# Kernel optimization log

Measured on AMD Instinct MI355X. Metric: run time of the kernel, lower is better.

## Reference

```python
import jax, jax.numpy as jnp
import numpy as np

H = 12
DH = 64
R = 8
LN_EPS = 1e-12


def setup_inputs() -> dict:
    key = jax.random.key(0)
    ks = jax.random.split(key, 6)
    B, T, D = 32, 512, 768
    s = 0.02  # realistic init scale so softmax/LN stay well-conditioned
    return {
        "hidden_states": jax.random.normal(ks[0], (B, T, D), jnp.float32),
        "Wq": jax.random.normal(ks[1], (D, D), jnp.float32) * s,
        "bq": jnp.zeros((D,), jnp.float32),
        "Wk": jax.random.normal(ks[2], (D, D), jnp.float32) * s,
        "bk": jnp.zeros((D,), jnp.float32),
        "Wv": jax.random.normal(ks[3], (D, D), jnp.float32) * s,
        "bv": jnp.zeros((D,), jnp.float32),
        "Wo": jax.random.normal(ks[4], (D, D), jnp.float32) * s,
        "bo": jnp.zeros((D,), jnp.float32),
        "ln_g": jnp.ones((D,), jnp.float32),
        "ln_b": jnp.zeros((D,), jnp.float32),
    }


def _bipartite_indices(metric, r):
    # metric: (B, T, dh); cosine-sim bipartite matching between even (a) and odd (b) tokens
    m = metric / (jnp.linalg.norm(metric, axis=-1, keepdims=True) + 1e-6)
    a, b = m[:, ::2], m[:, 1::2]
    scores = jnp.einsum('bad,bcd->bac', a, b)  # (B, Ta, Tb)
    node_max = scores.max(axis=-1)
    node_idx = scores.argmax(axis=-1)
    node_max = node_max.at[:, 0].set(-jnp.inf)  # protect CLS (a[0])
    r = min(r, a.shape[1] - 1)
    sorted_idx = jnp.argsort(-node_max, axis=-1)  # descending
    src_idx = sorted_idx[:, :r]
    unm_idx = sorted_idx[:, r:]
    dst_idx = jnp.take_along_axis(node_idx, src_idx, axis=-1)
    return src_idx, unm_idx, dst_idx


def _merge(x, src_idx, unm_idx, dst_idx):
    # x: (B, T, C) -> (B, T - r, C); scatter-mean matched even tokens into odd tokens
    src, dst = x[:, ::2], x[:, 1::2]
    matched = jnp.take_along_axis(src, src_idx[:, :, None], axis=1)  # (B, r, C)

    def scat(d, di, mm):
        sums = jnp.zeros_like(d).at[di].add(mm)
        cnt = jnp.zeros((d.shape[0],), d.dtype).at[di].add(jnp.ones(di.shape, d.dtype))
        # torch scatter_reduce 'mean' with include_self=True: (self + sum) / (1 + count)
        return (d + sums) / (1.0 + cnt[:, None])

    dst = jax.vmap(scat)(dst, dst_idx, matched)
    unm = jnp.take_along_axis(src, unm_idx[:, :, None], axis=1)
    return jnp.concatenate([unm, dst], axis=1)


def reference(hidden_states, Wq, bq, Wk, bk, Wv, bv, Wo, bo, ln_g, ln_b):
    B, T, D = hidden_states.shape

    def split_heads(x):
        return x.reshape(B, T, H, DH).transpose(0, 2, 1, 3)  # (B, H, T, dh)

    residual = hidden_states
    q = split_heads(hidden_states @ Wq + bq)
    k = split_heads(hidden_states @ Wk + bk)
    v = split_heads(hidden_states @ Wv + bv)

    # ToMe: match on head-averaged keys (computed under no_grad in torch)
    metric = jax.lax.stop_gradient(k.mean(axis=1))  # (B, T, dh)
    src_idx, unm_idx, dst_idx = _bipartite_indices(metric, R)

    def merge_heads(x):
        Bx, Hx, Tx, dx = x.shape
        y = x.transpose(0, 2, 1, 3).reshape(Bx, Tx, Hx * dx)
        y = _merge(y, src_idx, unm_idx, dst_idx)
        return y.reshape(Bx, y.shape[1], Hx, dx).transpose(0, 2, 1, 3)

    q = merge_heads(q)
    k = merge_heads(k)
    v = merge_heads(v)
    residual = _merge(residual, src_idx, unm_idx, dst_idx)

    scores = jnp.einsum('bhqd,bhkd->bhqk', q, k) / jnp.sqrt(jnp.float32(DH))
    probs = jax.nn.softmax(scores, axis=-1)  # dropout is identity in eval
    ctx = jnp.einsum('bhqk,bhkd->bhqd', probs, v)
    T2 = ctx.shape[2]
    ctx = ctx.transpose(0, 2, 1, 3).reshape(B, T2, D)
    out = ctx @ Wo + bo

    x = out + residual
    mu = x.mean(axis=-1, keepdims=True)
    var = x.var(axis=-1, keepdims=True)
    return (x - mu) / jnp.sqrt(var + LN_EPS) * ln_g + ln_b
```

## Files before the change

kernel.cpp:

```cpp
#include <hip/hip_runtime.h>
#include <math.h>

#define BNUM 32
#define TT   512
#define DD   768
#define HH   12
#define DHH  64
#define RR   8
#define TSRC 256
#define UNM  248
#define TM   504
#define MROW 16128

typedef unsigned short u16;
typedef unsigned int   u32;
typedef __attribute__((ext_vector_type(8))) short bfrag;
typedef __attribute__((ext_vector_type(4))) float ffrag;

__device__ __forceinline__ u16 f2bf(float f) {
  u32 u = __float_as_uint(f);
  u = (u + 0x7fffu + ((u >> 16) & 1u)) >> 16;
  return (u16)u;
}
__device__ __forceinline__ u32 pack2bf(float a, float b) {
  u32 ua = __float_as_uint(a), ub = __float_as_uint(b);
  ua += 0x7fffu + ((ua >> 16) & 1u);
  ub += 0x7fffu + ((ub >> 16) & 1u);
  return (ua >> 16) | (ub & 0xffff0000u);
}
__device__ __forceinline__ float bf2f(u16 v) {
  return __uint_as_float(((u32)v) << 16);
}

__device__ __forceinline__ void gl2lds16(const u16* g, u16* l) {
  __builtin_amdgcn_global_load_lds(
      (const __attribute__((address_space(1))) void*)(g),
      (__attribute__((address_space(3))) void*)(l), 16, 0, 0);
}

__global__ __launch_bounds__(256) void wkr_kernel(
    const float* __restrict__ Wk, const float* __restrict__ bk,
    float* __restrict__ Wkr, float* __restrict__ bkr) {
  int idx = blockIdx.x * 256 + threadIdx.x;
  int d = idx >> 6, j = idx & 63;
  float s = 0.f;
  #pragma unroll
  for (int h = 0; h < HH; ++h) s += Wk[(size_t)d * DD + h * DHH + j];
  Wkr[idx] = s * (1.f / 12.f);
  if (idx < 64) {
    float sb = 0.f;
    #pragma unroll
    for (int h = 0; h < HH; ++h) sb += bk[h * DHH + idx];
    bkr[idx] = sb * (1.f / 12.f);
  }
}

__global__ __launch_bounds__(256) void gemm_f32_kernel(
    const float* __restrict__ A, const float* __restrict__ W,
    const float* __restrict__ bias, float* __restrict__ C,
    int M, int N, int K) {
  __shared__ float As[32][34];
  __shared__ float Ws[32][66];
  const int t  = threadIdx.x;
  const int m0 = blockIdx.x * 32;
  const int tx = t & 15, ty = t >> 4;
  const int a_kk = t & 31;
  const int a_m  = t >> 5;
  const int w_n  = t & 63;
  const int w_k0 = t >> 6;

  float a_pre[4], w_pre[8];
  #pragma unroll
  for (int l = 0; l < 4; ++l)
    a_pre[l] = A[(size_t)(m0 + a_m + 8 * l) * K + a_kk];
  #pragma unroll
  for (int l = 0; l < 8; ++l)
    w_pre[l] = W[(size_t)(w_k0 * 8 + l) * N + w_n];

  float4 acc0 = make_float4(0.f, 0.f, 0.f, 0.f);
  float4 acc1 = make_float4(0.f, 0.f, 0.f, 0.f);

  for (int k0 = 0; k0 < K; k0 += 32) {
    __syncthreads();
    #pragma unroll
    for (int l = 0; l < 4; ++l) As[a_kk][a_m + 8 * l] = a_pre[l];
    #pragma unroll
    for (int l = 0; l < 8; ++l) Ws[w_k0 * 8 + l][w_n] = w_pre[l];
    __syncthreads();
    if (k0 + 32 < K) {
      #pragma unroll
      for (int l = 0; l < 4; ++l)
        a_pre[l] = A[(size_t)(m0 + a_m + 8 * l) * K + k0 + 32 + a_kk];
      #pragma unroll
      for (int l = 0; l < 8; ++l)
        w_pre[l] = W[(size_t)(k0 + 32 + w_k0 * 8 + l) * N + w_n];
    }
    #pragma unroll
    for (int kk = 0; kk < 32; ++kk) {
      float2 a2 = *(const float2*)&As[kk][ty * 2];
      float4 w4 = *(const float4*)&Ws[kk][tx * 4];
      acc0.x += a2.x * w4.x; acc0.y += a2.x * w4.y; acc0.z += a2.x * w4.z; acc0.w += a2.x * w4.w;
      acc1.x += a2.y * w4.x; acc1.y += a2.y * w4.y; acc1.z += a2.y * w4.z; acc1.w += a2.y * w4.w;
    }
  }
  const float4 b4 = *(const float4*)&bias[tx * 4];
  float4 v0 = acc0, v1 = acc1;
  v0.x += b4.x; v0.y += b4.y; v0.z += b4.z; v0.w += b4.w;
  v1.x += b4.x; v1.y += b4.y; v1.z += b4.z; v1.w += b4.w;
  *(float4*)&C[(size_t)(m0 + ty * 2) * N + tx * 4]     = v0;
  *(float4*)&C[(size_t)(m0 + ty * 2 + 1) * N + tx * 4] = v1;
}

__global__ __launch_bounds__(256) void wconv_kernel(
    const float* __restrict__ W0, const float* __restrict__ W1,
    const float* __restrict__ W2, const float* __restrict__ W3,
    u16* __restrict__ T0, u16* __restrict__ T1,
    u16* __restrict__ T2, u16* __restrict__ T3) {
  __shared__ float tile[64][65];
  int wi = blockIdx.z;
  const float* W = (wi == 0) ? W0 : (wi == 1) ? W1 : (wi == 2) ? W2 : W3;
  u16* T = (wi == 0) ? T0 : (wi == 1) ? T1 : (wi == 2) ? T2 : T3;
  int k0 = blockIdx.x * 64, n0 = blockIdx.y * 64;
  int t = threadIdx.x;
  int r = t >> 2, c4 = (t & 3) * 16;
  #pragma unroll
  for (int j = 0; j < 16; j += 4) {
    float4 v = *(const float4*)&W[(size_t)(k0 + r) * DD + n0 + c4 + j];
    tile[r][c4 + j] = v.x; tile[r][c4 + j + 1] = v.y;
    tile[r][c4 + j + 2] = v.z; tile[r][c4 + j + 3] = v.w;
  }
  __syncthreads();
  #pragma unroll
  for (int j = 0; j < 16; j += 2) {
    u32 p = (u32)f2bf(tile[c4 + j][r]) | ((u32)f2bf(tile[c4 + j + 1][r]) << 16);
    *(u32*)&T[(size_t)(n0 + r) * DD + k0 + c4 + j] = p;
  }
}

template <bool OUT_BF16, bool ADD_RES, bool ROW_BIAS, bool QK>
__global__ __launch_bounds__(256, 4) void mfma_gemm_kernel(
    const u16* __restrict__ A, const u16* __restrict__ BT,
    const float* __restrict__ bias, const float* __restrict__ bias2,
    const float* __restrict__ Res,
    float* __restrict__ Cf, u16* __restrict__ Cb, u16* __restrict__ Cb2,
    int M, int N, int K) {
  __shared__ u16 Als[2][128 * 32];
  __shared__ u16 Bls[2][128 * 32];
  const int t  = threadIdx.x;
  const int m0 = blockIdx.x * 128;
  const int n0 = blockIdx.y * 128;
  const int lane = t & 63;
  const int w  = t >> 6;
  const int wm = w & 1, wn = w >> 1;
  const int q  = lane >> 4;
  const int lr = lane & 15;

  const int srow = lane >> 2;
  const int schk = (lane & 3) ^ ((lane >> 3) & 3);
  const u16* gA = A  + (size_t)(m0 + w * 32 + srow) * K + schk * 8;
  const u16* gB = BT + (size_t)(n0 + w * 32 + srow) * K + schk * 8;

  const int ceff = q ^ ((lr >> 1) & 3);

  const float* biasp = bias;
  u16* Cbp = Cb;
  int n0c = n0;
  if (QK && n0 >= DD) { biasp = bias2; Cbp = Cb2; n0c = n0 - DD; }

  ffrag acc[4][4];
  #pragma unroll
  for (int i = 0; i < 4; ++i)
    #pragma unroll
    for (int j = 0; j < 4; ++j) {
      acc[i][j].x = 0.f; acc[i][j].y = 0.f; acc[i][j].z = 0.f; acc[i][j].w = 0.f;
    }

  auto STAGE = [&](int buf, int k0) {
    #pragma unroll
    for (int i = 0; i < 2; ++i) {
      gl2lds16(gA + (size_t)(i * 16) * K + k0, &Als[buf][(w * 32 + i * 16) * 32]);
      gl2lds16(gB + (size_t)(i * 16) * K + k0, &Bls[buf][(w * 32 + i * 16) * 32]);
    }
  };

  STAGE(0, 0);
  __syncthreads();

  const int NK = K >> 5;
  for (int kt = 0; kt < NK; ++kt) {
    const int cur = kt & 1;
    if (kt + 1 < NK) STAGE(cur ^ 1, (kt + 1) << 5);

    bfrag af[4], bfv[4];
    #pragma unroll
    for (int mi = 0; mi < 4; ++mi)
      af[mi] = *(const bfrag*)&Als[cur][((wm * 4 + mi) * 64 + lr * 4 + ceff) * 8];
    #pragma unroll
    for (int ni = 0; ni < 4; ++ni)
      bfv[ni] = *(const bfrag*)&Bls[cur][((wn * 4 + ni) * 64 + lr * 4 + ceff) * 8];
    #pragma unroll
    for (int mi = 0; mi < 4; ++mi)
      #pragma unroll
      for (int ni = 0; ni < 4; ++ni)
        acc[mi][ni] = __builtin_amdgcn_mfma_f32_16x16x32_bf16(
            af[mi], bfv[ni], acc[mi][ni], 0, 0, 0);

    __syncthreads();
  }

  float bcol[4];
  if (!ROW_BIAS) {
    #pragma unroll
    for (int ni = 0; ni < 4; ++ni)
      bcol[ni] = biasp[n0c + wn * 64 + ni * 16 + lr];
  }

  #pragma unroll
  for (int mi = 0; mi < 4; ++mi) {
    #pragma unroll
    for (int ni = 0; ni < 4; ++ni) {
      int gcol = n0c + wn * 64 + ni * 16 + lr;
      #pragma unroll
      for (int r = 0; r < 4; ++r) {
        int grow = m0 + wm * 64 + mi * 16 + q * 4 + r;
        size_t off = (size_t)grow * N + gcol;
        float v = acc[mi][ni][r];
        v += ROW_BIAS ? bias[grow] : bcol[ni];
        if (ADD_RES) v += Res[off];
        if (OUT_BF16) Cbp[off] = f2bf(v);
        else          Cf[off] = v;
      }
    }
  }
}

__global__ __launch_bounds__(256) void tome_kernel(
    const float* __restrict__ metric, int* __restrict__ order_g,
    int* __restrict__ dst_g) {
  __shared__ float sm[TSRC * 64];
  int b = blockIdx.x, i = threadIdx.x;
  const float* Mb = metric + (size_t)b * TT * 64;

  float areg[64];
  float na = 0.f;
  #pragma unroll
  for (int d = 0; d < 64; ++d) {
    float v = Mb[(size_t)(2 * i) * 64 + d];
    areg[d] = v; na += v * v;
  }
  float ia = 1.f / (sqrtf(na) + 1e-6f);
  #pragma unroll
  for (int d = 0; d < 64; ++d) areg[d] *= ia;

  float nb = 0.f;
  #pragma unroll
  for (int d = 0; d < 64; ++d) {
    float v = Mb[(size_t)(2 * i + 1) * 64 + d];
    sm[i * 64 + d] = v; nb += v * v;
  }
  float ib = 1.f / (sqrtf(nb) + 1e-6f);
  #pragma unroll
  for (int d = 0; d < 64; ++d) sm[i * 64 + d] *= ib;
  __syncthreads();

  float best = -INFINITY; int besti = 0;
  for (int c = 0; c < TSRC; ++c) {
    float s = 0.f;
    #pragma unroll
    for (int d = 0; d < 64; ++d) s += areg[d] * sm[c * 64 + d];
    if (s > best) { best = s; besti = c; }
  }
  if (i == 0) best = -INFINITY;
  __syncthreads();

  sm[i] = best;
  int* smi = (int*)(sm + TSRC);
  smi[i] = besti;
  __syncthreads();

  float ki = sm[i];
  int r = 0;
  for (int j = 0; j < TSRC; ++j) {
    float kj = sm[j];
    if (kj > ki || (kj == ki && j < i)) ++r;
  }
  int* ord = smi + TSRC;
  ord[r] = i;
  __syncthreads();

  order_g[b * TSRC + i] = ord[i];
  if (i < RR) dst_g[b * RR + i] = smi[ord[i]];
}

__global__ __launch_bounds__(256) void merge_kernel(
    const float* __restrict__ X, const int* __restrict__ order,
    const int* __restrict__ dsti, float* __restrict__ Xm,
    u16* __restrict__ Xmb) {
  int row = blockIdx.x;
  int b = row / TM, t2 = row % TM;
  int c = threadIdx.x;
  const float* Xb = X + (size_t)b * TT * DD;
  float out[3];
  if (t2 < UNM) {
    int tok = 2 * order[b * TSRC + RR + t2];
    #pragma unroll
    for (int l = 0; l < 3; ++l) out[l] = Xb[(size_t)tok * DD + c + 256 * l];
  } else {
    int j = t2 - UNM;
    float cnt = 1.f;
    #pragma unroll
    for (int l = 0; l < 3; ++l) out[l] = Xb[(size_t)(2 * j + 1) * DD + c + 256 * l];
    for (int m = 0; m < RR; ++m) {
      if (dsti[b * RR + m] == j) {
        int tok = 2 * order[b * TSRC + m];
        #pragma unroll
        for (int l = 0; l < 3; ++l) out[l] += Xb[(size_t)tok * DD + c + 256 * l];
        cnt += 1.f;
      }
    }
    float inv = 1.f / cnt;
    #pragma unroll
    for (int l = 0; l < 3; ++l) out[l] *= inv;
  }
  #pragma unroll
  for (int l = 0; l < 3; ++l) {
    Xm[(size_t)row * DD + c + 256 * l]  = out[l];
    Xmb[(size_t)row * DD + c + 256 * l] = f2bf(out[l]);
  }
}

#define NQT 8
__global__ __launch_bounds__(256) void attn_kernel(
    const u16* __restrict__ Q, const u16* __restrict__ K,
    const u16* __restrict__ VT, u16* __restrict__ ctx) {
  __shared__ u16 Kls[2][64][64];
  __shared__ u16 Vls[2][64][64];
  __shared__ u16 Pt[64][72];

  int blk = blockIdx.x;
  int bh = blk % (BNUM * HH);
  int qt = blk / (BNUM * HH);
  int h = bh % HH, b = bh / HH;
  const int t = threadIdx.x;
  const int lane = t & 63, w = t >> 6;
  const int lr = lane & 15, quad = lane >> 4;
  const int q0 = qt * 64;
  const size_t base = (size_t)b * TM * DD + (size_t)h * DHH;

  bfrag qf[2];
  {
    const u16* qp = Q + base + (size_t)(q0 + 16 * w + lr) * DD + quad * 8;
    qf[0] = *(const bfrag*)(qp);
    qf[1] = *(const bfrag*)(qp + 32);
  }

  const int srow = lane >> 3;
  const int schk = (lane & 7) ^ srow;
  const u16* Kg = K + base + (size_t)schk * 8;
  const u16* Vg0 = VT + (size_t)(h * DHH + w * 16 + srow) * MROW + (size_t)b * TM;
  const u16* Vg1 = Vg0 + (size_t)8 * MROW;

  const int cA = (quad)     ^ (lr & 7);
  const int cB = (quad + 4) ^ (lr & 7);

  float m_i = -INFINITY, l_i = 0.f;
  ffrag o[4];
  #pragma unroll
  for (int ni = 0; ni < 4; ++ni) {
    o[ni].x = 0.f; o[ni].y = 0.f; o[ni].z = 0.f; o[ni].w = 0.f;
  }

  auto STAGE = [&](int cur, int kt) {
    const int k0s = kt * 64;
    int t0 = k0s + w * 16 + srow;
    int t1 = t0 + 8;
    t0 = (t0 < TM) ? t0 : (TM - 1);
    t1 = (t1 < TM) ? t1 : (TM - 1);
    gl2lds16(Kg + (size_t)t0 * DD, &Kls[cur][w * 16][0]);
    gl2lds16(Kg + (size_t)t1 * DD, &Kls[cur][w * 16 + 8][0]);
    int tb = k0s + schk * 8;
    tb = (tb <= TM - 8) ? tb : (TM - 8);
    gl2lds16(Vg0 + tb, &Vls[cur][w * 16][0]);
    gl2lds16(Vg1 + tb, &Vls[cur][w * 16 + 8][0]);
  };

  STAGE(0, 0);
  __syncthreads();

  const float L2E = 1.4426950408889634f;
  const float C1  = 0.125f * 1.4426950408889634f;

  #pragma unroll
  for (int kt = 0; kt < NQT; ++kt) {
    const int cur = kt & 1;

    if (kt + 1 < NQT) STAGE(cur ^ 1, kt + 1);

    ffrag s4[4];
    __builtin_amdgcn_s_setprio(1);
    #pragma unroll
    for (int mi = 0; mi < 4; ++mi) {
      bfrag ka0 = *(const bfrag*)&Kls[cur][mi * 16 + lr][cA * 8];
      bfrag ka1 = *(const bfrag*)&Kls[cur][mi * 16 + lr][cB * 8];
      ffrag z; z.x = 0.f; z.y = 0.f; z.z = 0.f; z.w = 0.f;
      z = __builtin_amdgcn_mfma_f32_16x16x32_bf16(ka0, qf[0], z, 0, 0, 0);
      s4[mi] = __builtin_amdgcn_mfma_f32_16x16x32_bf16(ka1, qf[1], z, 0, 0, 0);
    }
    __builtin_amdgcn_s_setprio(0);

    if (kt == NQT - 1) {
      #pragma unroll
      for (int mi = 0; mi < 4; ++mi)
        #pragma unroll
        for (int r = 0; r < 4; ++r) {
          int rel = mi * 16 + quad * 4 + r;
          if (mi == 3)
            s4[mi][r] = (448 + rel < TM) ? s4[mi][r] : -INFINITY;
        }
    }

    float mx01 = fmaxf(fmaxf(s4[0][0], s4[0][1]), fmaxf(s4[0][2], s4[0][3]));
    float mx23 = fmaxf(fmaxf(s4[1][0], s4[1][1]), fmaxf(s4[1][2], s4[1][3]));
    float mx45 = fmaxf(fmaxf(s4[2][0], s4[2][1]), fmaxf(s4[2][2], s4[2][3]));
    float mx67 = fmaxf(fmaxf(s4[3][0], s4[3][1]), fmaxf(s4[3][2], s4[3][3]));
    float rmax = fmaxf(fmaxf(mx01, mx23), fmaxf(mx45, mx67));
    rmax = fmaxf(rmax, __shfl_xor(rmax, 16));
    rmax = fmaxf(rmax, __shfl_xor(rmax, 32));
    float nm = fmaxf(m_i, rmax * 0.125f);
    float alpha = __builtin_amdgcn_exp2f((m_i - nm) * L2E);
    float nml2 = nm * L2E;

    float p[16];
    float pa0 = 0.f, pa1 = 0.f, pa2 = 0.f, pa3 = 0.f;
    #pragma unroll
    for (int mi = 0; mi < 4; ++mi)
      #pragma unroll
      for (int r = 0; r < 4; ++r) {
        float e = __builtin_amdgcn_exp2f(__builtin_fmaf(s4[mi][r], C1, -nml2));
        p[mi * 4 + r] = e;
        if (r == 0) pa0 += e; else if (r == 1) pa1 += e;
        else if (r == 2) pa2 += e; else pa3 += e;
      }
    float psum = (pa0 + pa1) + (pa2 + pa3);
    psum += __shfl_xor(psum, 16);
    psum += __shfl_xor(psum, 32);
    l_i = l_i * alpha + psum;
    m_i = nm;

    #pragma unroll
    for (int mi = 0; mi < 4; ++mi) {
      u32 lo = pack2bf(p[mi * 4 + 0], p[mi * 4 + 1]);
      u32 hi = pack2bf(p[mi * 4 + 2], p[mi * 4 + 3]);
      u32* dst = (u32*)&Pt[16 * w + lr][mi * 16 + quad * 4];
      dst[0] = lo; dst[1] = hi;
    }

    float al[4];
    #pragma unroll
    for (int r = 0; r < 4; ++r) al[r] = __shfl(alpha, quad * 4 + r);
    #pragma unroll
    for (int ni = 0; ni < 4; ++ni)
      #pragma unroll
      for (int r = 0; r < 4; ++r) o[ni][r] *= al[r];

    bfrag pfa0 = *(const bfrag*)&Pt[16 * w + lr][quad * 8];
    bfrag pfa1 = *(const bfrag*)&Pt[16 * w + lr][32 + quad * 8];
    __builtin_amdgcn_s_setprio(1);
    #pragma unroll
    for (int ni = 0; ni < 4; ++ni) {
      bfrag vb0 = *(const bfrag*)&Vls[cur][ni * 16 + lr][cA * 8];
      bfrag vb1 = *(const bfrag*)&Vls[cur][ni * 16 + lr][cB * 8];
      o[ni] = __builtin_amdgcn_mfma_f32_16x16x32_bf16(pfa0, vb0, o[ni], 0, 0, 0);
      o[ni] = __builtin_amdgcn_mfma_f32_16x16x32_bf16(pfa1, vb1, o[ni], 0, 0, 0);
    }
    __builtin_amdgcn_s_setprio(0);

    __syncthreads();
  }

  float invl[4];
  #pragma unroll
  for (int r = 0; r < 4; ++r) {
    float lv = __shfl(l_i, quad * 4 + r);
    invl[r] = 1.f / lv;
  }
  #pragma unroll
  for (int r = 0; r < 4; ++r) {
    int row = q0 + 16 * w + quad * 4 + r;
    if (row < TM) {
      size_t g = base + (size_t)row * DD + lr;
      #pragma unroll
      for (int ni = 0; ni < 4; ++ni)
        ctx[g + ni * 16] = f2bf(o[ni][r] * invl[r]);
    }
  }
}

__global__ __launch_bounds__(256) void ln_kernel(
    float* __restrict__ Y, const float* __restrict__ g,
    const float* __restrict__ beta) {
  __shared__ float red[4];
  int row = blockIdx.x, t = threadIdx.x;
  size_t baseo = (size_t)row * DD;
  float x[3];
  #pragma unroll
  for (int l = 0; l < 3; ++l) x[l] = Y[baseo + t + 256 * l];
  float s = x[0] + x[1] + x[2];
  #pragma unroll
  for (int off = 32; off > 0; off >>= 1) s += __shfl_down(s, off, 64);
  if ((t & 63) == 0) red[t >> 6] = s;
  __syncthreads();
  float mu = (red[0] + red[1] + red[2] + red[3]) * (1.f / 768.f);
  __syncthreads();
  float d0 = x[0] - mu, d1 = x[1] - mu, d2 = x[2] - mu;
  float sq = d0 * d0 + d1 * d1 + d2 * d2;
  #pragma unroll
  for (int off = 32; off > 0; off >>= 1) sq += __shfl_down(sq, off, 64);
  if ((t & 63) == 0) red[t >> 6] = sq;
  __syncthreads();
  float var = (red[0] + red[1] + red[2] + red[3]) * (1.f / 768.f);
  float inv = rsqrtf(var + 1e-12f);
  #pragma unroll
  for (int l = 0; l < 3; ++l) {
    int c = t + 256 * l;
    Y[baseo + c] = (x[l] - mu) * inv * g[c] + beta[c];
  }
}

extern "C" void kernel_launch(void* const* d_in, const int* in_sizes, int n_in,
                              void* d_out, int out_size, void* d_ws, size_t ws_size,
                              hipStream_t stream) {
  const float* X    = (const float*)d_in[0];
  const float* Wq   = (const float*)d_in[1];
  const float* bq   = (const float*)d_in[2];
  const float* Wk   = (const float*)d_in[3];
  const float* bk   = (const float*)d_in[4];
  const float* Wv   = (const float*)d_in[5];
  const float* bv   = (const float*)d_in[6];
  const float* Wo   = (const float*)d_in[7];
  const float* bo   = (const float*)d_in[8];
  const float* ln_g = (const float*)d_in[9];
  const float* ln_b = (const float*)d_in[10];
  float* out = (float*)d_out;

  const size_t metric_n = (size_t)16384 * 64;
  const size_t wkr_n    = (size_t)768 * 64 + 64;
  const size_t idx_n    = (size_t)BNUM * TSRC + BNUM * RR;
  const size_t buf_n    = (size_t)MROW * DD;
  const size_t w_n      = (size_t)DD * DD;
  const size_t f32_elems = metric_n + wkr_n + idx_n + buf_n;
  const size_t u16_elems = 4 * buf_n + 4 * w_n;
  const size_t needed = f32_elems * 4 + u16_elems * 2;
  if (ws_size < needed) return;

  float* ws = (float*)d_ws;
  float* metric  = ws;
  float* Wkr     = metric + metric_n;
  float* bkr     = Wkr + (size_t)768 * 64;
  int*   order_g = (int*)(bkr + 64);
  int*   dst_g   = order_g + BNUM * TSRC;
  float* Xm      = (float*)(dst_g + BNUM * RR);
  u16*   Xmb     = (u16*)(Xm + buf_n);
  u16*   Qmb     = Xmb + buf_n;
  u16*   Kmb     = Qmb + buf_n;
  u16*   VTb     = Kmb + buf_n;
  u16*   WqT     = VTb + buf_n;
  u16*   WkT     = WqT + w_n;
  u16*   WvT     = WkT + w_n;
  u16*   WoT     = WvT + w_n;
  u16*   ctxb    = Qmb;

  wkr_kernel<<<(768 * 64) / 256, 256, 0, stream>>>(Wk, bk, Wkr, bkr);
  wconv_kernel<<<dim3(12, 12, 4), 256, 0, stream>>>(
      Wq, Wk, Wv, Wo, WqT, WkT, WvT, WoT);
  gemm_f32_kernel<<<dim3(16384 / 32, 1), 256, 0, stream>>>(
      X, Wkr, bkr, metric, 16384, 64, 768);
  tome_kernel<<<BNUM, 256, 0, stream>>>(metric, order_g, dst_g);
  merge_kernel<<<MROW, 256, 0, stream>>>(X, order_g, dst_g, Xm, Xmb);
  mfma_gemm_kernel<true, false, false, true>
      <<<dim3(MROW / 128, 2 * DD / 128), 256, 0, stream>>>(
      Xmb, WqT, bq, bk, nullptr, nullptr, Qmb, Kmb, MROW, DD, DD);
  mfma_gemm_kernel<true, false, true, false>
      <<<dim3(DD / 128, MROW / 128), 256, 0, stream>>>(
      WvT, Xmb, bv, nullptr, nullptr, nullptr, VTb, nullptr, DD, MROW, DD);
  attn_kernel<<<BNUM * HH * NQT, 256, 0, stream>>>(Qmb, Kmb, VTb, ctxb);
  mfma_gemm_kernel<false, true, false, false>
      <<<dim3(MROW / 128, DD / 128), 256, 0, stream>>>(
      ctxb, WoT, bo, nullptr, Xm, out, nullptr, nullptr, MROW, DD, DD);
  ln_kernel<<<MROW, 256, 0, stream>>>(out, ln_g, ln_b);
}
```

Before: 458.9 us.

## Split ToMe scoring across blocks, enlarge metric GEMM tile, remap MFMA grid, lazy softmax rescale

The ToMe matching kernel is split into a scoring kernel spread over 8 blocks per batch, with a shuffle argmax, and a separate ranking kernel. Before, only 32 blocks ran one long serial loop each. The fp32 metric GEMM now computes a 4x4 tile per thread over 64 rows. MFMA GEMM blocks are remapped so consecutive tiles land on the same XCD for better L2 reuse. Attention skips the online-softmax rescale unless the row max grows by more than a threshold, which saves exp and multiply work but lets probabilities be unnormalised by up to e^8 before the final divide.

New measurement: 398.7 us. -13.1%, faster.

```diff
diff --git a/kernel.cpp b/kernel.cpp
--- a/kernel.cpp
+++ b/kernel.cpp
@@ -59,37 +59,40 @@
     const float* __restrict__ A, const float* __restrict__ W,
     const float* __restrict__ bias, float* __restrict__ C,
     int M, int N, int K) {
-  __shared__ float As[32][34];
-  __shared__ float Ws[32][66];
+  __shared__ float As[32][68];
+  __shared__ float Ws[32][68];
   const int t  = threadIdx.x;
-  const int m0 = blockIdx.x * 32;
+  const int m0 = blockIdx.x * 64;
   const int tx = t & 15, ty = t >> 4;
   const int a_kk = t & 31;
   const int a_m  = t >> 5;
   const int w_n  = t & 63;
   const int w_k0 = t >> 6;
 
-  float a_pre[4], w_pre[8];
-  #pragma unroll
-  for (int l = 0; l < 4; ++l)
+  float a_pre[8], w_pre[8];
+  #pragma unroll
+  for (int l = 0; l < 8; ++l)
     a_pre[l] = A[(size_t)(m0 + a_m + 8 * l) * K + a_kk];
   #pragma unroll
   for (int l = 0; l < 8; ++l)
     w_pre[l] = W[(size_t)(w_k0 * 8 + l) * N + w_n];
 
-  float4 acc0 = make_float4(0.f, 0.f, 0.f, 0.f);
-  float4 acc1 = make_float4(0.f, 0.f, 0.f, 0.f);
+  float acc[4][4];
+  #pragma unroll
+  for (int i = 0; i < 4; ++i)
+    #pragma unroll
+    for (int j = 0; j < 4; ++j) acc[i][j] = 0.f;
 
   for (int k0 = 0; k0 < K; k0 += 32) {
     __syncthreads();
     #pragma unroll
-    for (int l = 0; l < 4; ++l) As[a_kk][a_m + 8 * l] = a_pre[l];
+    for (int l = 0; l < 8; ++l) As[a_kk][a_m + 8 * l] = a_pre[l];
     #pragma unroll
     for (int l = 0; l < 8; ++l) Ws[w_k0 * 8 + l][w_n] = w_pre[l];
     __syncthreads();
     if (k0 + 32 < K) {
       #pragma unroll
-      for (int l = 0; l < 4; ++l)
+      for (int l = 0; l < 8; ++l)
         a_pre[l] = A[(size_t)(m0 + a_m + 8 * l) * K + k0 + 32 + a_kk];
       #pragma unroll
       for (int l = 0; l < 8; ++l)
@@ -97,18 +100,26 @@
     }
     #pragma unroll
     for (int kk = 0; kk < 32; ++kk) {
-      float2 a2 = *(const float2*)&As[kk][ty * 2];
+      float4 a4 = *(const float4*)&As[kk][ty * 4];
       float4 w4 = *(const float4*)&Ws[kk][tx * 4];
-      acc0.x += a2.x * w4.x; acc0.y += a2.x * w4.y; acc0.z += a2.x * w4.z; acc0.w += a2.x * w4.w;
-      acc1.x += a2.y * w4.x; acc1.y += a2.y * w4.y; acc1.z += a2.y * w4.z; acc1.w += a2.y * w4.w;
+      acc[0][0] += a4.x * w4.x; acc[0][1] += a4.x * w4.y;
+      acc[0][2] += a4.x * w4.z; acc[0][3] += a4.x * w4.w;
+      acc[1][0] += a4.y * w4.x; acc[1][1] += a4.y * w4.y;
+      acc[1][2] += a4.y * w4.z; acc[1][3] += a4.y * w4.w;
+      acc[2][0] += a4.z * w4.x; acc[2][1] += a4.z * w4.y;
+      acc[2][2] += a4.z * w4.z; acc[2][3] += a4.z * w4.w;
+      acc[3][0] += a4.w * w4.x; acc[3][1] += a4.w * w4.y;
+      acc[3][2] += a4.w * w4.z; acc[3][3] += a4.w * w4.w;
     }
   }
   const float4 b4 = *(const float4*)&bias[tx * 4];
-  float4 v0 = acc0, v1 = acc1;
-  v0.x += b4.x; v0.y += b4.y; v0.z += b4.z; v0.w += b4.w;
-  v1.x += b4.x; v1.y += b4.y; v1.z += b4.z; v1.w += b4.w;
-  *(float4*)&C[(size_t)(m0 + ty * 2) * N + tx * 4]     = v0;
-  *(float4*)&C[(size_t)(m0 + ty * 2 + 1) * N + tx * 4] = v1;
+  #pragma unroll
+  for (int i = 0; i < 4; ++i) {
+    float4 v;
+    v.x = acc[i][0] + b4.x; v.y = acc[i][1] + b4.y;
+    v.z = acc[i][2] + b4.z; v.w = acc[i][3] + b4.w;
+    *(float4*)&C[(size_t)(m0 + ty * 4 + i) * N + tx * 4] = v;
+  }
 }
 
 __global__ __launch_bounds__(256) void wconv_kernel(
@@ -147,8 +158,18 @@
   __shared__ u16 Als[2][128 * 32];
   __shared__ u16 Bls[2][128 * 32];
   const int t  = threadIdx.x;
-  const int m0 = blockIdx.x * 128;
-  const int n0 = blockIdx.y * 128;
+
+  const int nwg = gridDim.x * gridDim.y;
+  int id = blockIdx.x + blockIdx.y * gridDim.x;
+  {
+    const int qq = nwg >> 3, rr = nwg & 7;
+    const int xcd = id & 7, pos = id >> 3;
+    id = (xcd < rr) ? (xcd * (qq + 1) + pos)
+                    : (rr * (qq + 1) + (xcd - rr) * qq + pos);
+  }
+  const int m0 = (id % gridDim.x) * 128;
+  const int n0 = (id / gridDim.x) * 128;
+
   const int lane = t & 63;
   const int w  = t >> 6;
   const int wm = w & 1, wn = w >> 1;
@@ -234,62 +255,96 @@
   }
 }
 
-__global__ __launch_bounds__(256) void tome_kernel(
-    const float* __restrict__ metric, int* __restrict__ order_g,
-    int* __restrict__ dst_g) {
-  __shared__ float sm[TSRC * 64];
-  int b = blockIdx.x, i = threadIdx.x;
+__global__ __launch_bounds__(256) void tome_scores_kernel(
+    const float* __restrict__ metric, float* __restrict__ node_max,
+    int* __restrict__ node_idx) {
+  __shared__ float Bs[128][68];
+  const int blk = blockIdx.x;
+  const int b = blk >> 3, g = blk & 7;
+  const int t = threadIdx.x;
+  const int r = t >> 3, cc = t & 7;
+  const int arow = g * 32 + r;
   const float* Mb = metric + (size_t)b * TT * 64;
 
   float areg[64];
   float na = 0.f;
   #pragma unroll
-  for (int d = 0; d < 64; ++d) {
-    float v = Mb[(size_t)(2 * i) * 64 + d];
-    areg[d] = v; na += v * v;
+  for (int d4 = 0; d4 < 16; ++d4) {
+    float4 v = *(const float4*)&Mb[(size_t)(2 * arow) * 64 + d4 * 4];
+    areg[4 * d4 + 0] = v.x; areg[4 * d4 + 1] = v.y;
+    areg[4 * d4 + 2] = v.z; areg[4 * d4 + 3] = v.w;
+    na += v.x * v.x; na += v.y * v.y; na += v.z * v.z; na += v.w * v.w;
   }
   float ia = 1.f / (sqrtf(na) + 1e-6f);
   #pragma unroll
   for (int d = 0; d < 64; ++d) areg[d] *= ia;
 
-  float nb = 0.f;
-  #pragma unroll
-  for (int d = 0; d < 64; ++d) {
-    float v = Mb[(size_t)(2 * i + 1) * 64 + d];
-    sm[i * 64 + d] = v; nb += v * v;
-  }
-  float ib = 1.f / (sqrtf(nb) + 1e-6f);
-  #pragma unroll
-  for (int d = 0; d < 64; ++d) sm[i * 64 + d] *= ib;
-  __syncthreads();
-
   float best = -INFINITY; int besti = 0;
-  for (int c = 0; c < TSRC; ++c) {
-    float s = 0.f;
-    #pragma unroll
-    for (int d = 0; d < 64; ++d) s += areg[d] * sm[c * 64 + d];
-    if (s > best) { best = s; besti = c; }
-  }
-  if (i == 0) best = -INFINITY;
-  __syncthreads();
-
-  sm[i] = best;
-  int* smi = (int*)(sm + TSRC);
-  smi[i] = besti;
-  __syncthreads();
-
-  float ki = sm[i];
+  for (int p = 0; p < 2; ++p) {
+    __syncthreads();
+    if (t < 128) {
+      int c = p * 128 + t;
+      const float* src = &Mb[(size_t)(2 * c + 1) * 64];
+      float nb = 0.f;
+      #pragma unroll
+      for (int d4 = 0; d4 < 16; ++d4) {
+        float4 v = *(const float4*)&src[d4 * 4];
+        *(float4*)&Bs[t][d4 * 4] = v;
+        nb += v.x * v.x; nb += v.y * v.y; nb += v.z * v.z; nb += v.w * v.w;
+      }
+      float ib = 1.f / (sqrtf(nb) + 1e-6f);
+      #pragma unroll
+      for (int d4 = 0; d4 < 16; ++d4) {
+        float4 v = *(float4*)&Bs[t][d4 * 4];
+        v.x *= ib; v.y *= ib; v.z *= ib; v.w *= ib;
+        *(float4*)&Bs[t][d4 * 4] = v;
+      }
+    }
+    __syncthreads();
+    for (int j = 0; j < 16; ++j) {
+      int cl = cc + 8 * j;
+      float s = 0.f;
+      #pragma unroll
+      for (int d4 = 0; d4 < 16; ++d4) {
+        float4 bv = *(const float4*)&Bs[cl][d4 * 4];
+        s += areg[4 * d4 + 0] * bv.x; s += areg[4 * d4 + 1] * bv.y;
+        s += areg[4 * d4 + 2] * bv.z; s += areg[4 * d4 + 3] * bv.w;
+      }
+      int c = p * 128 + cl;
+      if (s > best) { best = s; besti = c; }
+    }
+  }
+  #pragma unroll
+  for (int off = 1; off < 8; off <<= 1) {
+    float bm = __shfl_xor(best, off);
+    int   bi = __shfl_xor(besti, off);
+    if (bm > best || (bm == best && bi < besti)) { best = bm; besti = bi; }
+  }
+  if (cc == 0) {
+    node_max[b * TSRC + arow] = best;
+    node_idx[b * TSRC + arow] = besti;
+  }
+}
+
+__global__ __launch_bounds__(256) void tome_rank_kernel(
+    const float* __restrict__ node_max, const int* __restrict__ node_idx,
+    int* __restrict__ order_g, int* __restrict__ dst_g) {
+  __shared__ float km[TSRC];
+  __shared__ int ord[TSRC];
+  int b = blockIdx.x, i = threadIdx.x;
+  float best = (i == 0) ? -INFINITY : node_max[b * TSRC + i];
+  km[i] = best;
+  __syncthreads();
+  float ki = km[i];
   int r = 0;
   for (int j = 0; j < TSRC; ++j) {
-    float kj = sm[j];
+    float kj = km[j];
     if (kj > ki || (kj == ki && j < i)) ++r;
   }
-  int* ord = smi + TSRC;
   ord[r] = i;
   __syncthreads();
-
   order_g[b * TSRC + i] = ord[i];
-  if (i < RR) dst_g[b * RR + i] = smi[ord[i]];
+  if (i < RR) dst_g[b * RR + i] = node_idx[b * TSRC + ord[i]];
 }
 
 __global__ __launch_bounds__(256) void merge_kernel(
@@ -426,9 +481,22 @@
     float rmax = fmaxf(fmaxf(mx01, mx23), fmaxf(mx45, mx67));
     rmax = fmaxf(rmax, __shfl_xor(rmax, 16));
     rmax = fmaxf(rmax, __shfl_xor(rmax, 32));
-    float nm = fmaxf(m_i, rmax * 0.125f);
-    float alpha = __builtin_amdgcn_exp2f((m_i - nm) * L2E);
-    float nml2 = nm * L2E;
+    float pmax = rmax * 0.125f;
+
+    if (!__all(pmax <= m_i + 8.f)) {
+      float nm = fmaxf(m_i, pmax);
+      float alpha = __builtin_amdgcn_exp2f((m_i - nm) * L2E);
+      float al[4];
+      #pragma unroll
+      for (int r = 0; r < 4; ++r) al[r] = __shfl(alpha, quad * 4 + r);
+      #pragma unroll
+      for (int ni = 0; ni < 4; ++ni)
+        #pragma unroll
+        for (int r = 0; r < 4; ++r) o[ni][r] *= al[r];
+      l_i *= alpha;
+      m_i = nm;
+    }
+    float nml2 = m_i * L2E;
 
     float p[16];
     float pa0 = 0.f, pa1 = 0.f, pa2 = 0.f, pa3 = 0.f;
@@ -444,8 +512,7 @@
     float psum = (pa0 + pa1) + (pa2 + pa3);
     psum += __shfl_xor(psum, 16);
     psum += __shfl_xor(psum, 32);
-    l_i = l_i * alpha + psum;
-    m_i = nm;
+    l_i += psum;
 
     #pragma unroll
     for (int mi = 0; mi < 4; ++mi) {
@@ -454,14 +521,6 @@
       u32* dst = (u32*)&Pt[16 * w + lr][mi * 16 + quad * 4];
       dst[0] = lo; dst[1] = hi;
     }
-
-    float al[4];
-    #pragma unroll
-    for (int r = 0; r < 4; ++r) al[r] = __shfl(alpha, quad * 4 + r);
-    #pragma unroll
-    for (int ni = 0; ni < 4; ++ni)
-      #pragma unroll
-      for (int r = 0; r < 4; ++r) o[ni][r] *= al[r];
 
     bfrag pfa0 = *(const bfrag*)&Pt[16 * w + lr][quad * 8];
     bfrag pfa1 = *(const bfrag*)&Pt[16 * w + lr][32 + quad * 8];
@@ -546,36 +605,40 @@
   const size_t metric_n = (size_t)16384 * 64;
   const size_t wkr_n    = (size_t)768 * 64 + 64;
   const size_t idx_n    = (size_t)BNUM * TSRC + BNUM * RR;
+  const size_t nm_n     = (size_t)2 * BNUM * TSRC;
   const size_t buf_n    = (size_t)MROW * DD;
   const size_t w_n      = (size_t)DD * DD;
-  const size_t f32_elems = metric_n + wkr_n + idx_n + buf_n;
+  const size_t f32_elems = metric_n + wkr_n + idx_n + nm_n + buf_n;
   const size_t u16_elems = 4 * buf_n + 4 * w_n;
   const size_t needed = f32_elems * 4 + u16_elems * 2;
   if (ws_size < needed) return;
 
   float* ws = (float*)d_ws;
-  float* metric  = ws;
-  float* Wkr     = metric + metric_n;
-  float* bkr     = Wkr + (size_t)768 * 64;
-  int*   order_g = (int*)(bkr + 64);
-  int*   dst_g   = order_g + BNUM * TSRC;
-  float* Xm      = (float*)(dst_g + BNUM * RR);
-  u16*   Xmb     = (u16*)(Xm + buf_n);
-  u16*   Qmb     = Xmb + buf_n;
-  u16*   Kmb     = Qmb + buf_n;
-  u16*   VTb     = Kmb + buf_n;
-  u16*   WqT     = VTb + buf_n;
-  u16*   WkT     = WqT + w_n;
-  u16*   WvT     = WkT + w_n;
-  u16*   WoT     = WvT + w_n;
-  u16*   ctxb    = Qmb;
+  float* metric   = ws;
+  float* Wkr      = metric + metric_n;
+  float* bkr      = Wkr + (size_t)768 * 64;
+  int*   order_g  = (int*)(bkr + 64);
+  int*   dst_g    = order_g + BNUM * TSRC;
+  float* node_max = (float*)(dst_g + BNUM * RR);
+  int*   node_idx = (int*)(node_max + BNUM * TSRC);
+  float* Xm       = (float*)(node_idx + BNUM * TSRC);
+  u16*   Xmb      = (u16*)(Xm + buf_n);
+  u16*   Qmb      = Xmb + buf_n;
+  u16*   Kmb      = Qmb + buf_n;
+  u16*   VTb      = Kmb + buf_n;
+  u16*   WqT      = VTb + buf_n;
+  u16*   WkT      = WqT + w_n;
+  u16*   WvT      = WkT + w_n;
+  u16*   WoT      = WvT + w_n;
+  u16*   ctxb     = Qmb;
 
   wkr_kernel<<<(768 * 64) / 256, 256, 0, stream>>>(Wk, bk, Wkr, bkr);
   wconv_kernel<<<dim3(12, 12, 4), 256, 0, stream>>>(
       Wq, Wk, Wv, Wo, WqT, WkT, WvT, WoT);
-  gemm_f32_kernel<<<dim3(16384 / 32, 1), 256, 0, stream>>>(
+  gemm_f32_kernel<<<dim3(16384 / 64, 1), 256, 0, stream>>>(
       X, Wkr, bkr, metric, 16384, 64, 768);
-  tome_kernel<<<BNUM, 256, 0, stream>>>(metric, order_g, dst_g);
+  tome_scores_kernel<<<BNUM * 8, 256, 0, stream>>>(metric, node_max, node_idx);
+  tome_rank_kernel<<<BNUM, 256, 0, stream>>>(node_max, node_idx, order_g, dst_g);
   merge_kernel<<<MROW, 256, 0, stream>>>(X, order_g, dst_g, Xm, Xmb);
   mfma_gemm_kernel<true, false, false, true>
       <<<dim3(MROW / 128, 2 * DD / 128), 256, 0, stream>>>(
```
